# Performance work log

Measured on AMD Instinct MI355X. Metric: run time of the kernel, lower is better.

## Reference

```python
import jax, jax.numpy as jnp
import numpy as np

B, S, HID = 4, 2048, 2048
NH, NKV, HD = 16, 4, 128  # head_dim = HID // NH
Q_SIZE, KV_SIZE = NH * HD, NKV * HD


def setup_inputs() -> dict:
    key = jax.random.key(0)
    ks = jax.random.split(key, 8)
    pos = jnp.arange(S, dtype=jnp.float32)[:, None]
    inv_freq = 1.0 / (10000.0 ** (jnp.arange(0, HD, 2, dtype=jnp.float32) / HD))  # [HD/2]
    ang = pos * inv_freq[None, :]  # [S, HD/2]
    return {
        "hidden_states": jax.random.normal(ks[0], (B, S, HID), jnp.float32),
        "rotary_pos_emb_cos": jnp.cos(ang),
        "rotary_pos_emb_sin": jnp.sin(ang),
        "w_qkv": jax.random.normal(ks[1], (HID, Q_SIZE + 2 * KV_SIZE), jnp.float32) * (HID ** -0.5),
        "b_qkv": jax.random.normal(ks[2], (Q_SIZE + 2 * KV_SIZE,), jnp.float32) * 0.02,
        "w_o": jax.random.normal(ks[3], (HID, HID), jnp.float32) * (HID ** -0.5),
        "b_o": jax.random.normal(ks[4], (HID,), jnp.float32) * 0.02,
    }


def _apply_rope(x, cos, sin):
    # x: [B, S, H, D]; cos/sin: [S, D/2]; rotate-half (non-interleaved) convention
    d2 = x.shape[-1] // 2
    x1, x2 = x[..., :d2], x[..., d2:]
    c = cos[None, :, None, :]
    s = sin[None, :, None, :]
    return jnp.concatenate([x1 * c - x2 * s, x2 * c + x1 * s], axis=-1)


def reference(hidden_states, rotary_pos_emb_cos, rotary_pos_emb_sin, w_qkv, b_qkv, w_o, b_o):
    b, s, _ = hidden_states.shape
    qkv = hidden_states @ w_qkv + b_qkv  # [B, S, Q_SIZE + 2*KV_SIZE]
    q, k, v = jnp.split(qkv, [Q_SIZE, Q_SIZE + KV_SIZE], axis=-1)
    q = q.reshape(b, s, NH, HD)
    k = k.reshape(b, s, NKV, HD)
    v = v.reshape(b, s, NKV, HD)
    q = _apply_rope(q, rotary_pos_emb_cos, rotary_pos_emb_sin)
    k = _apply_rope(k, rotary_pos_emb_cos, rotary_pos_emb_sin)
    # grouped-query attention: repeat kv heads to match query heads
    g = NH // NKV
    k = jnp.repeat(k, g, axis=2)  # [B, S, NH, HD]
    v = jnp.repeat(v, g, axis=2)
    scale = HD ** -0.5
    scores = jnp.einsum("bshd,bthd->bhst", q, k) * scale  # [B, NH, S, S]
    probs = jax.nn.softmax(scores, axis=-1)
    out = jnp.einsum("bhst,bthd->bshd", probs, v)  # [B, S, NH, HD]
    out = out.reshape(b, s, NH * HD)
    return out @ w_o + b_o
```

## Files before the change

kernel.cpp:

```cpp
#include <hip/hip_runtime.h>
#include <math.h>

#define B_N   4
#define S_N   2048
#define HID_N 2048
#define NH_N  16
#define NKV_N 4
#define HD_N  128
#define QSZ   2048
#define KVSZ  512
#define QKVN  3072
#define M_N   8192

typedef __bf16 bf16;
typedef __bf16 bf16x8 __attribute__((ext_vector_type(8)));
typedef float  f32x4  __attribute__((ext_vector_type(4)));

#define GLL16(gp, lp)                                                          \
  __builtin_amdgcn_global_load_lds(                                            \
      (const __attribute__((address_space(1))) void*)(gp),                     \
      (__attribute__((address_space(3))) void*)(lp), 16, 0, 0)

__device__ __forceinline__ f32x4 mfma16(bf16x8 a, bf16x8 b, f32x4 c) {
  return __builtin_amdgcn_mfma_f32_16x16x32_bf16(a, b, c, 0, 0, 0);
}

__global__ __launch_bounds__(256) void conv_bf16_kernel(
    const float* __restrict__ X, bf16* __restrict__ Y)
{
  size_t i = ((size_t)blockIdx.x * 256 + threadIdx.x) * 8;
  float4 a = *(const float4*)&X[i];
  float4 b = *(const float4*)&X[i + 4];
  union { bf16 h[8]; uint4 u; } pk;
  pk.h[0] = (bf16)a.x; pk.h[1] = (bf16)a.y; pk.h[2] = (bf16)a.z; pk.h[3] = (bf16)a.w;
  pk.h[4] = (bf16)b.x; pk.h[5] = (bf16)b.y; pk.h[6] = (bf16)b.z; pk.h[7] = (bf16)b.w;
  *(uint4*)&Y[i] = pk.u;
}

__global__ __launch_bounds__(256) void convT_kernel(
    const float* __restrict__ W, bf16* __restrict__ Wt, int K, int N)
{
  __shared__ __attribute__((aligned(16))) bf16 tile[64 * 68];
  const int n0 = blockIdx.x * 64, k0 = blockIdx.y * 64;
#pragma unroll
  for (int it = 0; it < 4; ++it) {
    int idx = it * 256 + threadIdx.x;
    int r = idx >> 4, c4 = (idx & 15) << 2;
    float4 v = *(const float4*)&W[(size_t)(k0 + r) * N + n0 + c4];
    union { bf16 h[4]; unsigned long long u; } pk;
    pk.h[0] = (bf16)v.x; pk.h[1] = (bf16)v.y; pk.h[2] = (bf16)v.z; pk.h[3] = (bf16)v.w;
    *(unsigned long long*)&tile[r * 68 + c4] = pk.u;
  }
  __syncthreads();
#pragma unroll
  for (int it = 0; it < 4; ++it) {
    int idx = it * 256 + threadIdx.x;
    int rn = idx >> 4, ck4 = (idx & 15) << 2;
    union { bf16 h[4]; unsigned long long u; } pk;
#pragma unroll
    for (int i = 0; i < 4; ++i) pk.h[i] = tile[(ck4 + i) * 68 + rn];
    *(unsigned long long*)&Wt[(size_t)(n0 + rn) * K + k0 + ck4] = pk.u;
  }
}

template <bool OUT_BF16>
__global__ __launch_bounds__(256, 2) void gemm_bf16_kernel(
    const bf16* __restrict__ A, const bf16* __restrict__ Bt,
    const float* __restrict__ bias, void* __restrict__ Cout,
    int M, int N, int K)
{
  __shared__ __attribute__((aligned(16))) bf16 As[128 * 32];
  __shared__ __attribute__((aligned(16))) bf16 Bs[128 * 32];

  const int tid  = threadIdx.x;
  const int lane = tid & 63, wv = tid >> 6;
  const int quad = lane >> 4, ln = lane & 15;
  const int row0 = blockIdx.y * 128, col0 = blockIdx.x * 128;
  const int wr = (wv >> 1) * 64, wc = (wv & 1) * 64;

  f32x4 acc[4][4];
  const f32x4 zero = {0.f, 0.f, 0.f, 0.f};
#pragma unroll
  for (int mt = 0; mt < 4; ++mt)
#pragma unroll
    for (int nt = 0; nt < 4; ++nt) acc[mt][nt] = zero;

  const int s0 = wv * 128 + lane;
  const bf16* gA0 = A  + (size_t)(row0 + (s0 >> 2)) * K + (s0 & 3) * 8;
  const bf16* gA1 = gA0 + 16 * (size_t)K;
  const bf16* gB0 = Bt + (size_t)(col0 + (s0 >> 2)) * K + (s0 & 3) * 8;
  const bf16* gB1 = gB0 + 16 * (size_t)K;
  bf16* lA0 = As + (size_t)wv * 1024;
  bf16* lA1 = lA0 + 512;
  bf16* lB0 = Bs + (size_t)wv * 1024;
  bf16* lB1 = lB0 + 512;

  for (int k0 = 0; k0 < K; k0 += 32) {
    GLL16(gA0 + k0, lA0);
    GLL16(gA1 + k0, lA1);
    GLL16(gB0 + k0, lB0);
    GLL16(gB1 + k0, lB1);
    __syncthreads();

    bf16x8 a[4], b[4];
#pragma unroll
    for (int mt = 0; mt < 4; ++mt)
      a[mt] = *(const bf16x8*)&As[(wr + mt * 16 + ln) * 32 + quad * 8];
#pragma unroll
    for (int nt = 0; nt < 4; ++nt)
      b[nt] = *(const bf16x8*)&Bs[(wc + nt * 16 + ln) * 32 + quad * 8];
#pragma unroll
    for (int mt = 0; mt < 4; ++mt)
#pragma unroll
      for (int nt = 0; nt < 4; ++nt)
        acc[mt][nt] = mfma16(a[mt], b[nt], acc[mt][nt]);
    __syncthreads();
  }

#pragma unroll
  for (int nt = 0; nt < 4; ++nt) {
    const int c = col0 + wc + nt * 16 + ln;
    const float bv = bias[c];
#pragma unroll
    for (int mt = 0; mt < 4; ++mt) {
#pragma unroll
      for (int r = 0; r < 4; ++r) {
        const int rr = row0 + wr + mt * 16 + quad * 4 + r;
        const float v = acc[mt][nt][r] + bv;
        if (OUT_BF16) ((bf16*)Cout)[(size_t)rr * N + c] = (bf16)v;
        else          ((float*)Cout)[(size_t)rr * N + c] = v;
      }
    }
  }
}

__global__ __launch_bounds__(256) void rope_repack_kernel(
    const bf16* __restrict__ qkvB, const float* __restrict__ cosb,
    const float* __restrict__ sinb, bf16* __restrict__ Qb, bf16* __restrict__ Kb)
{
  int idx = blockIdx.x * 256 + threadIdx.x;
  int j  = idx & 63;
  int m  = (idx >> 6) & (M_N - 1);
  int hh = idx >> 19;
  int b = m >> 11, s = m & (S_N - 1);
  float c  = cosb[s * 64 + j];
  float sn = sinb[s * 64 + j];
  if (hh < NH_N) {
    const bf16* src = qkvB + (size_t)m * QKVN + hh * HD_N;
    float x1 = (float)src[j], x2 = (float)src[j + 64];
    bf16* dst = Qb + ((size_t)(b * NH_N + hh) * S_N + s) * HD_N;
    const float qs = 0.08838834764831845f * 1.4426950408889634f;
    dst[j]      = (bf16)((x1 * c - x2 * sn) * qs);
    dst[j + 64] = (bf16)((x2 * c + x1 * sn) * qs);
  } else {
    int kh = hh - NH_N;
    const bf16* src = qkvB + (size_t)m * QKVN + QSZ + kh * HD_N;
    float x1 = (float)src[j], x2 = (float)src[j + 64];
    bf16* dst = Kb + ((size_t)(b * NKV_N + kh) * S_N + s) * HD_N;
    dst[j]      = (bf16)(x1 * c - x2 * sn);
    dst[j + 64] = (bf16)(x2 * c + x1 * sn);
  }
}

__global__ __launch_bounds__(256) void transposeV_kernel(
    const bf16* __restrict__ qkvB, bf16* __restrict__ Vt)
{
  __shared__ __attribute__((aligned(16))) bf16 tile[64 * 136];
  const int s0 = blockIdx.x * 64;
  const int bkh = blockIdx.y;
  const int b = bkh >> 2, kh = bkh & 3;
#pragma unroll
  for (int it = 0; it < 4; ++it) {
    int ci = it * 256 + threadIdx.x;
    int r = ci >> 4, c = ci & 15;
    uint4 v = *(const uint4*)&qkvB[(size_t)(b * S_N + s0 + r) * QKVN +
                                   QSZ + KVSZ + kh * HD_N + c * 8];
    *(uint4*)&tile[r * 136 + c * 8] = v;
  }
  __syncthreads();
#pragma unroll
  for (int it = 0; it < 4; ++it) {
    int ci = it * 256 + threadIdx.x;
    int d = ci >> 3, c = ci & 7;
    union { bf16 h[8]; uint4 u; } pk;
#pragma unroll
    for (int i = 0; i < 8; ++i) pk.h[i] = tile[(c * 8 + i) * 136 + d];
    *(uint4*)&Vt[((size_t)bkh * HD_N + d) * S_N + s0 + c * 8] = pk.u;
  }
}

__global__ __launch_bounds__(256, 3) void attn_mfma_kernel(
    const bf16* __restrict__ Qb, const bf16* __restrict__ Kb,
    const bf16* __restrict__ Vt, bf16* __restrict__ Ob)
{
  __shared__ __attribute__((aligned(16))) bf16 Ks[64 * 128];
  __shared__ __attribute__((aligned(16))) bf16 Vs[128 * 64];
  __shared__ __attribute__((aligned(16))) bf16 Ps[64 * 72];

  const int tid  = threadIdx.x;
  const int lane = tid & 63, wv = tid >> 6;
  const int quad = lane >> 4, ln = lane & 15;
  const int q0 = blockIdx.x * 64;
  const int h  = blockIdx.y, b = blockIdx.z;
  const int kh = h >> 2;

  const bf16* Qg = Qb + ((size_t)(b * NH_N + h) * S_N + q0) * HD_N;
  const bf16* Kg = Kb + (size_t)(b * NKV_N + kh) * S_N * HD_N;
  const bf16* Vg = Vt + (size_t)(b * NKV_N + kh) * HD_N * S_N;

#pragma unroll
  for (int t = 0; t < 4; ++t) {
    int slot = (t * 4 + wv) * 64 + lane;
    int row = slot >> 4, cc = slot & 15;
    int csrc = (cc & 8) | ((cc & 7) ^ (row & 7));
    GLL16(Qg + row * 128 + csrc * 8, Ks + (size_t)(t * 4 + wv) * 512);
  }
  __syncthreads();
  bf16x8 aq[4];
  {
    const int q = wv * 16 + ln;
#pragma unroll
    for (int dc = 0; dc < 4; ++dc) {
      int c = dc * 4 + quad;
      int cs = (c & 8) | ((c & 7) ^ (q & 7));
      aq[dc] = *(const bf16x8*)&Ks[q * 128 + cs * 8];
    }
  }
  __syncthreads();

  bf16x8 bones;
#pragma unroll
  for (int j = 0; j < 8; ++j) bones[j] = (ln == 0) ? (bf16)1.0f : (bf16)0.0f;

  f32x4 accO[8];
  const f32x4 zero = {0.f, 0.f, 0.f, 0.f};
#pragma unroll
  for (int dt = 0; dt < 8; ++dt) accO[dt] = zero;
  f32x4 accL = zero;

  for (int kt = 0; kt < S_N; kt += 64) {
#pragma unroll
    for (int t = 0; t < 4; ++t) {
      int slot = (t * 4 + wv) * 64 + lane;
      int row = slot >> 4, cc = slot & 15;
      int csrc = (cc & 8) | ((cc & 7) ^ (row & 7));
      GLL16(Kg + (size_t)(kt + row) * 128 + csrc * 8,
            Ks + (size_t)(t * 4 + wv) * 512);
    }
#pragma unroll
    for (int t = 0; t < 4; ++t) {
      int slot = (t * 4 + wv) * 64 + lane;
      int row = slot >> 3, cc = slot & 7;
      int csrc = cc ^ (row & 7);
      GLL16(Vg + (size_t)row * S_N + kt + csrc * 8,
            Vs + (size_t)(t * 4 + wv) * 512);
    }
    __syncthreads();

    f32x4 accS[4];
#pragma unroll
    for (int nt = 0; nt < 4; ++nt) accS[nt] = zero;
#pragma unroll
    for (int nt = 0; nt < 4; ++nt) {
      const int kp = nt * 16 + ln;
#pragma unroll
      for (int dc = 0; dc < 4; ++dc) {
        int c = dc * 4 + quad;
        int cs = (c & 8) | ((c & 7) ^ (kp & 7));
        bf16x8 bk = *(const bf16x8*)&Ks[kp * 128 + cs * 8];
        accS[nt] = mfma16(aq[dc], bk, accS[nt]);
      }
    }

#pragma unroll
    for (int r = 0; r < 4; ++r) {
      const int q = wv * 16 + quad * 4 + r;
      Ps[q * 72 +  0 + ln] = (bf16)__builtin_amdgcn_exp2f(accS[0][r]);
      Ps[q * 72 + 16 + ln] = (bf16)__builtin_amdgcn_exp2f(accS[1][r]);
      Ps[q * 72 + 32 + ln] = (bf16)__builtin_amdgcn_exp2f(accS[2][r]);
      Ps[q * 72 + 48 + ln] = (bf16)__builtin_amdgcn_exp2f(accS[3][r]);
    }

    bf16x8 ap0 = *(const bf16x8*)&Ps[(wv * 16 + ln) * 72 + quad * 8];
    bf16x8 ap1 = *(const bf16x8*)&Ps[(wv * 16 + ln) * 72 + 32 + quad * 8];
    accL = mfma16(ap0, bones, accL);
    accL = mfma16(ap1, bones, accL);
#pragma unroll
    for (int dt = 0; dt < 8; ++dt) {
      const int d = dt * 16 + ln;
      {
        int cs = quad ^ (d & 7);
        bf16x8 bv = *(const bf16x8*)&Vs[d * 64 + cs * 8];
        accO[dt] = mfma16(ap0, bv, accO[dt]);
      }
      {
        int cs = (4 + quad) ^ (d & 7);
        bf16x8 bv = *(const bf16x8*)&Vs[d * 64 + cs * 8];
        accO[dt] = mfma16(ap1, bv, accO[dt]);
      }
    }
    __syncthreads();
  }

#pragma unroll
  for (int r = 0; r < 4; ++r) {
    const float l = __shfl(accL[r], lane & 48);
    const float inv = 1.f / l;
    const int q = q0 + wv * 16 + quad * 4 + r;
    const size_t base = ((size_t)b * S_N + q) * HID_N + h * HD_N;
#pragma unroll
    for (int dt = 0; dt < 8; ++dt)
      Ob[base + dt * 16 + ln] = (bf16)(accO[dt][r] * inv);
  }
}

extern "C" void kernel_launch(void* const* d_in, const int* in_sizes, int n_in,
                              void* d_out, int out_size, void* d_ws, size_t ws_size,
                              hipStream_t stream) {
  const float* hidden = (const float*)d_in[0];
  const float* cosb   = (const float*)d_in[1];
  const float* sinb   = (const float*)d_in[2];
  const float* w_qkv  = (const float*)d_in[3];
  const float* b_qkv  = (const float*)d_in[4];
  const float* w_o    = (const float*)d_in[5];
  const float* b_o    = (const float*)d_in[6];
  float* out = (float*)d_out;

  char* w = (char*)d_ws;
  bf16* qkvB  = (bf16*)(w);
  bf16* Qb    = (bf16*)(w + 50331648);
  bf16* Kb    = (bf16*)(w + 83886080);
  bf16* Vt    = (bf16*)(w + 92274688);
  bf16* wqkvT = (bf16*)(w + 100663296);
  bf16* woT   = (bf16*)(w + 113246208);
  bf16* hidB  = (bf16*)(w + 121634816);
  bf16* attnB = hidB;

  conv_bf16_kernel<<<(M_N * HID_N) / (256 * 8), 256, 0, stream>>>(hidden, hidB);
  convT_kernel<<<dim3(QKVN / 64, HID_N / 64), 256, 0, stream>>>(w_qkv, wqkvT, HID_N, QKVN);
  convT_kernel<<<dim3(HID_N / 64, HID_N / 64), 256, 0, stream>>>(w_o, woT, HID_N, HID_N);

  gemm_bf16_kernel<true><<<dim3(QKVN / 128, M_N / 128), 256, 0, stream>>>(
      hidB, wqkvT, b_qkv, qkvB, M_N, QKVN, HID_N);

  rope_repack_kernel<<<(M_N * (NH_N + NKV_N) * 64) / 256, 256, 0, stream>>>(
      qkvB, cosb, sinb, Qb, Kb);
  transposeV_kernel<<<dim3(S_N / 64, B_N * NKV_N), 256, 0, stream>>>(qkvB, Vt);

  attn_mfma_kernel<<<dim3(S_N / 64, NH_N, B_N), 256, 0, stream>>>(Qb, Kb, Vt, attnB);

  gemm_bf16_kernel<false><<<dim3(HID_N / 128, M_N / 128), 256, 0, stream>>>(
      attnB, woT, b_o, out, M_N, HID_N, HID_N);
}
```

Before: 568.9 us.

## Process two 64-row query tiles per attention block to reuse K/V tiles

Each attention workgroup now handles 128 query rows instead of 64, with each wave computing two 16-row query slices against the same K and V tiles loaded into shared memory. This halves the number of K/V global loads and LDS fills per query row and doubles the MFMA work per barrier. In exchange it doubles accumulator registers (two sets of output and score accumulators) and enlarges the P buffer, which may reduce occupancy under the 3-blocks launch bound and halves the grid size.

```diff
diff --git a/kernel.cpp b/kernel.cpp
--- a/kernel.cpp
+++ b/kernel.cpp
@@ -195,12 +195,12 @@
 {
   __shared__ __attribute__((aligned(16))) bf16 Ks[64 * 128];
   __shared__ __attribute__((aligned(16))) bf16 Vs[128 * 64];
-  __shared__ __attribute__((aligned(16))) bf16 Ps[64 * 72];
+  __shared__ __attribute__((aligned(16))) bf16 Ps[128 * 72];
 
   const int tid  = threadIdx.x;
   const int lane = tid & 63, wv = tid >> 6;
   const int quad = lane >> 4, ln = lane & 15;
-  const int q0 = blockIdx.x * 64;
+  const int q0 = blockIdx.x * 128;
   const int h  = blockIdx.y, b = blockIdx.z;
   const int kh = h >> 2;
 
@@ -214,16 +214,18 @@
     int row = slot >> 4, cc = slot & 15;
     int csrc = (cc & 8) | ((cc & 7) ^ (row & 7));
     GLL16(Qg + row * 128 + csrc * 8, Ks + (size_t)(t * 4 + wv) * 512);
+    GLL16(Qg + (64 + row) * 128 + csrc * 8, Vs + (size_t)(t * 4 + wv) * 512);
   }
   __syncthreads();
-  bf16x8 aq[4];
+  bf16x8 aq0[4], aq1[4];
   {
     const int q = wv * 16 + ln;
 #pragma unroll
     for (int dc = 0; dc < 4; ++dc) {
       int c = dc * 4 + quad;
       int cs = (c & 8) | ((c & 7) ^ (q & 7));
-      aq[dc] = *(const bf16x8*)&Ks[q * 128 + cs * 8];
+      aq0[dc] = *(const bf16x8*)&Ks[q * 128 + cs * 8];
+      aq1[dc] = *(const bf16x8*)&Vs[q * 128 + cs * 8];
     }
   }
   __syncthreads();
@@ -232,11 +234,11 @@
 #pragma unroll
   for (int j = 0; j < 8; ++j) bones[j] = (ln == 0) ? (bf16)1.0f : (bf16)0.0f;
 
-  f32x4 accO[8];
+  f32x4 accO0[8], accO1[8];
   const f32x4 zero = {0.f, 0.f, 0.f, 0.f};
 #pragma unroll
-  for (int dt = 0; dt < 8; ++dt) accO[dt] = zero;
-  f32x4 accL = zero;
+  for (int dt = 0; dt < 8; ++dt) { accO0[dt] = zero; accO1[dt] = zero; }
+  f32x4 accL0 = zero, accL1 = zero;
 
   for (int kt = 0; kt < S_N; kt += 64) {
 #pragma unroll
@@ -257,9 +259,9 @@
     }
     __syncthreads();
 
-    f32x4 accS[4];
-#pragma unroll
-    for (int nt = 0; nt < 4; ++nt) accS[nt] = zero;
+    f32x4 s0[4], s1[4];
+#pragma unroll
+    for (int nt = 0; nt < 4; ++nt) { s0[nt] = zero; s1[nt] = zero; }
 #pragma unroll
     for (int nt = 0; nt < 4; ++nt) {
       const int kp = nt * 16 + ln;
@@ -268,35 +270,44 @@
         int c = dc * 4 + quad;
         int cs = (c & 8) | ((c & 7) ^ (kp & 7));
         bf16x8 bk = *(const bf16x8*)&Ks[kp * 128 + cs * 8];
-        accS[nt] = mfma16(aq[dc], bk, accS[nt]);
+        s0[nt] = mfma16(aq0[dc], bk, s0[nt]);
+        s1[nt] = mfma16(aq1[dc], bk, s1[nt]);
       }
     }
 
 #pragma unroll
     for (int r = 0; r < 4; ++r) {
-      const int q = wv * 16 + quad * 4 + r;
-      Ps[q * 72 +  0 + ln] = (bf16)__builtin_amdgcn_exp2f(accS[0][r]);
-      Ps[q * 72 + 16 + ln] = (bf16)__builtin_amdgcn_exp2f(accS[1][r]);
-      Ps[q * 72 + 32 + ln] = (bf16)__builtin_amdgcn_exp2f(accS[2][r]);
-      Ps[q * 72 + 48 + ln] = (bf16)__builtin_amdgcn_exp2f(accS[3][r]);
-    }
-
-    bf16x8 ap0 = *(const bf16x8*)&Ps[(wv * 16 + ln) * 72 + quad * 8];
-    bf16x8 ap1 = *(const bf16x8*)&Ps[(wv * 16 + ln) * 72 + 32 + quad * 8];
-    accL = mfma16(ap0, bones, accL);
-    accL = mfma16(ap1, bones, accL);
+      const int qA = wv * 16 + quad * 4 + r;
+      const int qB = 64 + qA;
+#pragma unroll
+      for (int nt = 0; nt < 4; ++nt) {
+        Ps[qA * 72 + nt * 16 + ln] = (bf16)__builtin_amdgcn_exp2f(s0[nt][r]);
+        Ps[qB * 72 + nt * 16 + ln] = (bf16)__builtin_amdgcn_exp2f(s1[nt][r]);
+      }
+    }
+
+    bf16x8 apA0 = *(const bf16x8*)&Ps[(wv * 16 + ln) * 72 + quad * 8];
+    bf16x8 apA1 = *(const bf16x8*)&Ps[(wv * 16 + ln) * 72 + 32 + quad * 8];
+    bf16x8 apB0 = *(const bf16x8*)&Ps[(64 + wv * 16 + ln) * 72 + quad * 8];
+    bf16x8 apB1 = *(const bf16x8*)&Ps[(64 + wv * 16 + ln) * 72 + 32 + quad * 8];
+    accL0 = mfma16(apA0, bones, accL0);
+    accL0 = mfma16(apA1, bones, accL0);
+    accL1 = mfma16(apB0, bones, accL1);
+    accL1 = mfma16(apB1, bones, accL1);
 #pragma unroll
     for (int dt = 0; dt < 8; ++dt) {
       const int d = dt * 16 + ln;
       {
         int cs = quad ^ (d & 7);
         bf16x8 bv = *(const bf16x8*)&Vs[d * 64 + cs * 8];
-        accO[dt] = mfma16(ap0, bv, accO[dt]);
+        accO0[dt] = mfma16(apA0, bv, accO0[dt]);
+        accO1[dt] = mfma16(apB0, bv, accO1[dt]);
       }
       {
         int cs = (4 + quad) ^ (d & 7);
         bf16x8 bv = *(const bf16x8*)&Vs[d * 64 + cs * 8];
-        accO[dt] = mfma16(ap1, bv, accO[dt]);
+        accO0[dt] = mfma16(apA1, bv, accO0[dt]);
+        accO1[dt] = mfma16(apB1, bv, accO1[dt]);
       }
     }
     __syncthreads();
@@ -304,13 +315,19 @@
 
 #pragma unroll
   for (int r = 0; r < 4; ++r) {
-    const float l = __shfl(accL[r], lane & 48);
-    const float inv = 1.f / l;
-    const int q = q0 + wv * 16 + quad * 4 + r;
-    const size_t base = ((size_t)b * S_N + q) * HID_N + h * HD_N;
-#pragma unroll
-    for (int dt = 0; dt < 8; ++dt)
-      Ob[base + dt * 16 + ln] = (bf16)(accO[dt][r] * inv);
+    const float lA = __shfl(accL0[r], lane & 48);
+    const float lB = __shfl(accL1[r], lane & 48);
+    const float invA = 1.f / lA;
+    const float invB = 1.f / lB;
+    const int qA = q0 + wv * 16 + quad * 4 + r;
+    const int qB = qA + 64;
+    const size_t baseA = ((size_t)b * S_N + qA) * HID_N + h * HD_N;
+    const size_t baseB = ((size_t)b * S_N + qB) * HID_N + h * HD_N;
+#pragma unroll
+    for (int dt = 0; dt < 8; ++dt) {
+      Ob[baseA + dt * 16 + ln] = (bf16)(accO0[dt][r] * invA);
+      Ob[baseB + dt * 16 + ln] = (bf16)(accO1[dt][r] * invB);
+    }
   }
 }
 
@@ -347,7 +364,7 @@
       qkvB, cosb, sinb, Qb, Kb);
   transposeV_kernel<<<dim3(S_N / 64, B_N * NKV_N), 256, 0, stream>>>(qkvB, Vt);
 
-  attn_mfma_kernel<<<dim3(S_N / 64, NH_N, B_N), 256, 0, stream>>>(Qb, Kb, Vt, attnB);
+  attn_mfma_kernel<<<dim3(S_N / 128, NH_N, B_N), 256, 0, stream>>>(Qb, Kb, Vt, attnB);
 
   gemm_bf16_kernel<false><<<dim3(HID_N / 128, M_N / 128), 256, 0, stream>>>(
       attnB, woT, b_o, out, M_N, HID_N, HID_N);
```

New measurement: 620.4 us. 9.1% more time.
